# Optimization experiments

Hardware: AMD Instinct MI355X
Metric: run time of the kernel (lower is better)

The kernel has to match this reference:

```python
import jax, jax.numpy as jnp
import numpy as np


def _dF(field, c):
    """Central differences of component c of field [B,X,Y,Z,C] -> [B,X-2,Y-2,Z-2,3]."""
    f = field[..., c]
    dx = (f[:, 2:, 1:-1, 1:-1] - f[:, :-2, 1:-1, 1:-1]) * 0.5
    dy = (f[:, 1:-1, 2:, 1:-1] - f[:, 1:-1, :-2, 1:-1]) * 0.5
    dz = (f[:, 1:-1, 1:-1, 2:] - f[:, 1:-1, 1:-1, :-2]) * 0.5
    return jnp.stack((dx, dy, dz), axis=4)


def setup_inputs() -> dict:
    key = jax.random.key(0)
    grid = jax.random.normal(key, (2, 160, 160, 160, 3), dtype=jnp.float32)
    return {"grid": grid}


def reference(grid):
    # First derivatives of each displacement component: [B,X-2,Y-2,Z-2,3]
    dx = _dF(grid, 0)
    dy = _dF(grid, 1)
    dz = _dF(grid, 2)
    # Second derivatives: [B,X-4,Y-4,Z-4,3]
    dxx = _dF(dx, 0)
    dyy = _dF(dy, 1)
    dzz = _dF(dz, 2)
    dxy = _dF(dx, 1)
    dyz = _dF(dy, 2)
    dxz = _dF(dx, 2)
    penalty = jnp.sum(dxx ** 2 + dyy ** 2 + dzz ** 2
                      + 2.0 * (dxy ** 2 + dyz ** 2 + dxz ** 2))
    return penalty / dxx.size
```

## Files before the change

kernel.cpp:

```cpp
#include <hip/hip_runtime.h>

#define OY 480
#define OX 76800
#define SB 12288000
#define IT 12
#define NSEG 13
#define NBLK 1014
#define INV_SIZE (1.0f/22778496.0f)

#define ROW_SHL1 0x101
#define ROW_SHL2 0x102
#define ROW_SHR1 0x111
#define ROW_SHR2 0x112

template<int CTRL>
__device__ __forceinline__ float dppf(float x){
    return __int_as_float(__builtin_amdgcn_update_dpp(
        0, __float_as_int(x), CTRL, 0xF, 0xF, true));
}

__device__ __forceinline__ float4 ld4p(const float* p){ return *reinterpret_cast<const float4*>(p); }

#define STEP(P, V0a, V0b, DP, WC, WN) { \
    const int s = 2*d + (P); \
    if (qact) { \
        if (s <= 14) { \
            WN[0]=ld4p(nx);    WN[1]=ld4p(nx+4);  WN[2]=ld4p(nx+8); \
            WN[3]=ld4p(nx+12); WN[4]=ld4p(nx+16); WN[5]=ld4p(nx+20); \
            nx += OX; \
        } \
        float x[24]; \
        _Pragma("unroll") for (int q=0;q<6;++q){ \
            x[4*q]=WC[q].x; x[4*q+1]=WC[q].y; x[4*q+2]=WC[q].z; x[4*q+3]=WC[q].w; } \
        float dz0[4], dz1[4], dz2[4], dy0[4], dy1[4], v0c[4]; \
        _Pragma("unroll") for (int v=0; v<4; ++v) { \
            v0c[v] = x[3*v+6]; \
            dz0[v] = x[3*v+9]  - x[3*v+3]; \
            dz1[v] = x[3*v+10] - x[3*v+4]; \
            dz2[v] = x[3*v+11] - x[3*v+5]; \
            dy0[v] = dppf<ROW_SHR1>(x[3*v+6]) - dppf<ROW_SHL1>(x[3*v+6]); \
            dy1[v] = dppf<ROW_SHR1>(x[3*v+7]) - dppf<ROW_SHL1>(x[3*v+7]); \
        } \
        if (s >= 2 && s <= 13) { \
            _Pragma("unroll") for (int v=0; v<4; ++v) { \
                float c0 = x[3*v+6], c1 = x[3*v+7]; \
                float hy0 = dppf<ROW_SHR2>(c0) - 2.f*c0 + dppf<ROW_SHL2>(c0); \
                float hy1 = dppf<ROW_SHR2>(c1) - 2.f*c1 + dppf<ROW_SHL2>(c1); \
                float yz0 = dppf<ROW_SHR1>(dz0[v]) - dppf<ROW_SHL1>(dz0[v]); \
                float yz1 = dppf<ROW_SHR1>(dz1[v]) - dppf<ROW_SHL1>(dz1[v]); \
                float yz2 = dppf<ROW_SHR1>(dz2[v]) - dppf<ROW_SHL1>(dz2[v]); \
                if (vr) { \
                    float zz0 = x[3*v+12] - 2.f*x[3*v+6] + x[3*v]; \
                    float zz1 = x[3*v+13] - 2.f*x[3*v+7] + x[3*v+1]; \
                    float zz2 = x[3*v+14] - 2.f*x[3*v+8] + x[3*v+2]; \
                    cls2 = fmaf(zz0,zz0,cls2); cls2 = fmaf(zz1,zz1,cls2); cls1 = fmaf(zz2,zz2,cls1); \
                    cls2 = fmaf(hy0,hy0,cls2); cls1 = fmaf(hy1,hy1,cls1); \
                    cls4 = fmaf(yz0,yz0,cls4); cls3 = fmaf(yz1,yz1,cls3); cls1 = fmaf(yz2,yz2,cls1); \
                } \
            } \
        } \
        const bool eXY = vr && (s >= 3) && (s <= 14); \
        const bool eXX = vr && (s >= 4); \
        _Pragma("unroll") for (int v=0; v<4; ++v) { \
            if (eXY) { float h; \
                h = dy0[v] - DP[0][v]; cls3 = fmaf(h,h,cls3); \
                h = dy1[v] - DP[1][v]; cls1 = fmaf(h,h,cls1); \
                h = dz0[v] - DP[2][v]; cls3 = fmaf(h,h,cls3); \
                h = dz1[v] - DP[3][v]; cls2 = fmaf(h,h,cls2); \
                h = dz2[v] - DP[4][v]; cls1 = fmaf(h,h,cls1); \
            } \
            DP[0][v] = dy0[v]; DP[1][v] = dy1[v]; \
            DP[2][v] = dz0[v]; DP[3][v] = dz1[v]; DP[4][v] = dz2[v]; \
            if (eXX) { float h = v0c[v] - 2.f*V0a[v] + V0b[v]; cls1 = fmaf(h,h,cls1); } \
            V0b[v] = V0a[v]; V0a[v] = v0c[v]; \
        } \
    } \
}

__global__ __launch_bounds__(256)
void be_partials(const float* __restrict__ g, float* __restrict__ partial) {
    __shared__ float wsum[4];

    const int tid = threadIdx.x;
    const int bid = blockIdx.x;
    const int is = bid % NSEG;
    int r1 = bid / NSEG;
    const int zt = r1 % 3;  r1 /= 3;
    const int jt = r1 % 13;
    const int bb = r1 / 13;

    const int j0  = 2 + jt*12;
    const int zlo = 64*zt;
    const int i0  = 2 + is*IT;
    const float* __restrict__ G = g + (size_t)bb*SB + (size_t)(j0-2)*OY + 3*zlo;

    const int r = tid & 15;
    const int Q = tid >> 4;
    const int qmax = (zt == 2) ? 7 : 16;
    const bool qact = Q < qmax;
    const bool vr = (r >= 2) && (r <= 13);
    const float* lane0 = G + (size_t)r*OY + 12*Q;
    const float* nx = lane0 + (size_t)(i0-1)*OX;

    float4 wA[6], wB[6];
    float v0A0[4], v0A1[4], v0B0[4], v0B1[4];
    float dpA[5][4], dpB[5][4];
    #pragma unroll
    for (int v=0; v<4; ++v) {
        v0A0[v]=v0A1[v]=v0B0[v]=v0B1[v]=0.f;
        #pragma unroll
        for (int q=0; q<5; ++q) { dpA[q][v]=0.f; dpB[q][v]=0.f; }
    }
    float cls1=0.f, cls2=0.f, cls3=0.f, cls4=0.f;

    if (qact) {
        const float* wp = lane0 + (size_t)(i0-2)*OX;
        wA[0]=ld4p(wp);    wA[1]=ld4p(wp+4);  wA[2]=ld4p(wp+8);
        wA[3]=ld4p(wp+12); wA[4]=ld4p(wp+16); wA[5]=ld4p(wp+20);
    }

    #pragma unroll 1
    for (int d = 0; d < 8; ++d) {
        STEP(0, v0A0, v0A1, dpA, wA, wB)
        STEP(1, v0B0, v0B1, dpB, wB, wA)
    }

    float sv = fmaf(2.f, cls2, cls1);
    sv = fmaf(3.f, cls3, sv);
    sv = fmaf(4.f, cls4, sv);
    sv *= 0.0625f;

    #pragma unroll
    for (int off = 32; off > 0; off >>= 1) sv += __shfl_down(sv, off, 64);
    if ((tid & 63) == 0) wsum[tid >> 6] = sv;
    __syncthreads();
    if (tid == 0)
        partial[bid] = (wsum[0] + wsum[1]) + (wsum[2] + wsum[3]);
}

__global__ __launch_bounds__(256)
void be_final(const float* __restrict__ partial, float* __restrict__ out) {
    float s = 0.0f;
    for (int i = threadIdx.x; i < NBLK; i += 256) s += partial[i];
    #pragma unroll
    for (int off = 32; off > 0; off >>= 1) s += __shfl_down(s, off, 64);
    __shared__ float ws[4];
    if ((threadIdx.x & 63) == 0) ws[threadIdx.x >> 6] = s;
    __syncthreads();
    if (threadIdx.x == 0)
        out[0] = ((ws[0] + ws[1]) + (ws[2] + ws[3])) * INV_SIZE;
}

extern "C" void kernel_launch(void* const* d_in, const int* in_sizes, int n_in,
                              void* d_out, int out_size, void* d_ws, size_t ws_size,
                              hipStream_t stream) {
    const float* grid = (const float*)d_in[0];
    float* out = (float*)d_out;
    float* partials = (float*)d_ws;

    be_partials<<<dim3(NBLK), dim3(256), 0, stream>>>(grid, partials);
    be_final<<<1, 256, 0, stream>>>(partials, out);
}
```

Baseline: 166.8 us.

## Stage grid slices through triple-buffered LDS with coalesced loads in single-wave blocks

Each block becomes a single 64-thread wave over a narrower z-window, with 3380 blocks instead of 1014. Each X-slice is fetched with coalesced float4 loads, prefetched one slice ahead in registers and written into a three-slot LDS ring. The stencil then reads its overlapping 24-float windows from LDS rather than issuing redundant overlapping global loads. The slice loop is fully unrolled and the cross-wave shared-memory reduction is dropped. The design relies on in-order LDS access within one wavefront instead of barriers, and it adds LDS traffic plus a larger partials array.

```diff
diff --git a/kernel.cpp b/kernel.cpp
--- a/kernel.cpp
+++ b/kernel.cpp
@@ -3,9 +3,11 @@
 #define OY 480
 #define OX 76800
 #define SB 12288000
+#define RST 60
+#define SLC 960
 #define IT 12
 #define NSEG 13
-#define NBLK 1014
+#define NBLK 3380
 #define INV_SIZE (1.0f/22778496.0f)
 
 #define ROW_SHL1 0x101
@@ -20,90 +22,102 @@
 }
 
 __device__ __forceinline__ float4 ld4p(const float* p){ return *reinterpret_cast<const float4*>(p); }
+__device__ __forceinline__ void st4p(float* p, float4 v){ *reinterpret_cast<float4*>(p) = v; }
 
-#define STEP(P, V0a, V0b, DP, WC, WN) { \
-    const int s = 2*d + (P); \
+#define STEPX(S, V0a, V0b, DP, SBc, SBn) { \
+    if ((S) <= 13) { \
+        const float* bp = Gs + (size_t)((S)+2)*OX; \
+        SBn[0]=ld4p(bp+gof0); SBn[1]=ld4p(bp+gof1); SBn[2]=ld4p(bp+gof2); \
+        if (wv3) SBn[3]=ld4p(bp+gof3); \
+    } \
     if (qact) { \
-        if (s <= 14) { \
-            WN[0]=ld4p(nx);    WN[1]=ld4p(nx+4);  WN[2]=ld4p(nx+8); \
-            WN[3]=ld4p(nx+12); WN[4]=ld4p(nx+16); WN[5]=ld4p(nx+20); \
-            nx += OX; \
-        } \
+        const float* Lr = lds + ((S)%3)*SLC + oj; \
         float x[24]; \
-        _Pragma("unroll") for (int q=0;q<6;++q){ \
-            x[4*q]=WC[q].x; x[4*q+1]=WC[q].y; x[4*q+2]=WC[q].z; x[4*q+3]=WC[q].w; } \
-        float dz0[4], dz1[4], dz2[4], dy0[4], dy1[4], v0c[4]; \
+        { float4 y0=ld4p(Lr),y1=ld4p(Lr+4),y2=ld4p(Lr+8),y3=ld4p(Lr+12),y4=ld4p(Lr+16),y5=ld4p(Lr+20); \
+          x[0]=y0.x;x[1]=y0.y;x[2]=y0.z;x[3]=y0.w; x[4]=y1.x;x[5]=y1.y;x[6]=y1.z;x[7]=y1.w; \
+          x[8]=y2.x;x[9]=y2.y;x[10]=y2.z;x[11]=y2.w; x[12]=y3.x;x[13]=y3.y;x[14]=y3.z;x[15]=y3.w; \
+          x[16]=y4.x;x[17]=y4.y;x[18]=y4.z;x[19]=y4.w; x[20]=y5.x;x[21]=y5.y;x[22]=y5.z;x[23]=y5.w; } \
+        float dz0[4],dz1[4],dz2[4],dy0[4],dy1[4],v0c[4]; \
         _Pragma("unroll") for (int v=0; v<4; ++v) { \
             v0c[v] = x[3*v+6]; \
-            dz0[v] = x[3*v+9]  - x[3*v+3]; \
-            dz1[v] = x[3*v+10] - x[3*v+4]; \
-            dz2[v] = x[3*v+11] - x[3*v+5]; \
+            dz0[v] = x[3*v+9]-x[3*v+3]; dz1[v]=x[3*v+10]-x[3*v+4]; dz2[v]=x[3*v+11]-x[3*v+5]; \
             dy0[v] = dppf<ROW_SHR1>(x[3*v+6]) - dppf<ROW_SHL1>(x[3*v+6]); \
             dy1[v] = dppf<ROW_SHR1>(x[3*v+7]) - dppf<ROW_SHL1>(x[3*v+7]); \
         } \
-        if (s >= 2 && s <= 13) { \
+        if ((S) >= 2 && (S) <= 13) { \
             _Pragma("unroll") for (int v=0; v<4; ++v) { \
-                float c0 = x[3*v+6], c1 = x[3*v+7]; \
+                float c0=x[3*v+6], c1=x[3*v+7]; \
                 float hy0 = dppf<ROW_SHR2>(c0) - 2.f*c0 + dppf<ROW_SHL2>(c0); \
                 float hy1 = dppf<ROW_SHR2>(c1) - 2.f*c1 + dppf<ROW_SHL2>(c1); \
                 float yz0 = dppf<ROW_SHR1>(dz0[v]) - dppf<ROW_SHL1>(dz0[v]); \
                 float yz1 = dppf<ROW_SHR1>(dz1[v]) - dppf<ROW_SHL1>(dz1[v]); \
                 float yz2 = dppf<ROW_SHR1>(dz2[v]) - dppf<ROW_SHL1>(dz2[v]); \
                 if (vr) { \
-                    float zz0 = x[3*v+12] - 2.f*x[3*v+6] + x[3*v]; \
-                    float zz1 = x[3*v+13] - 2.f*x[3*v+7] + x[3*v+1]; \
-                    float zz2 = x[3*v+14] - 2.f*x[3*v+8] + x[3*v+2]; \
-                    cls2 = fmaf(zz0,zz0,cls2); cls2 = fmaf(zz1,zz1,cls2); cls1 = fmaf(zz2,zz2,cls1); \
-                    cls2 = fmaf(hy0,hy0,cls2); cls1 = fmaf(hy1,hy1,cls1); \
-                    cls4 = fmaf(yz0,yz0,cls4); cls3 = fmaf(yz1,yz1,cls3); cls1 = fmaf(yz2,yz2,cls1); \
+                    float zz0 = x[3*v+12]-2.f*x[3*v+6]+x[3*v]; \
+                    float zz1 = x[3*v+13]-2.f*x[3*v+7]+x[3*v+1]; \
+                    float zz2 = x[3*v+14]-2.f*x[3*v+8]+x[3*v+2]; \
+                    cls2=fmaf(zz0,zz0,cls2); cls2=fmaf(zz1,zz1,cls2); cls1=fmaf(zz2,zz2,cls1); \
+                    cls2=fmaf(hy0,hy0,cls2); cls1=fmaf(hy1,hy1,cls1); \
+                    cls4=fmaf(yz0,yz0,cls4); cls3=fmaf(yz1,yz1,cls3); cls1=fmaf(yz2,yz2,cls1); \
                 } \
             } \
         } \
-        const bool eXY = vr && (s >= 3) && (s <= 14); \
-        const bool eXX = vr && (s >= 4); \
         _Pragma("unroll") for (int v=0; v<4; ++v) { \
-            if (eXY) { float h; \
-                h = dy0[v] - DP[0][v]; cls3 = fmaf(h,h,cls3); \
-                h = dy1[v] - DP[1][v]; cls1 = fmaf(h,h,cls1); \
-                h = dz0[v] - DP[2][v]; cls3 = fmaf(h,h,cls3); \
-                h = dz1[v] - DP[3][v]; cls2 = fmaf(h,h,cls2); \
-                h = dz2[v] - DP[4][v]; cls1 = fmaf(h,h,cls1); \
+            if (vr && (S) >= 3 && (S) <= 14) { float h; \
+                h=dy0[v]-DP[0][v]; cls3=fmaf(h,h,cls3); \
+                h=dy1[v]-DP[1][v]; cls1=fmaf(h,h,cls1); \
+                h=dz0[v]-DP[2][v]; cls3=fmaf(h,h,cls3); \
+                h=dz1[v]-DP[3][v]; cls2=fmaf(h,h,cls2); \
+                h=dz2[v]-DP[4][v]; cls1=fmaf(h,h,cls1); \
             } \
-            DP[0][v] = dy0[v]; DP[1][v] = dy1[v]; \
-            DP[2][v] = dz0[v]; DP[3][v] = dz1[v]; DP[4][v] = dz2[v]; \
-            if (eXX) { float h = v0c[v] - 2.f*V0a[v] + V0b[v]; cls1 = fmaf(h,h,cls1); } \
-            V0b[v] = V0a[v]; V0a[v] = v0c[v]; \
+            DP[0][v]=dy0[v]; DP[1][v]=dy1[v]; DP[2][v]=dz0[v]; DP[3][v]=dz1[v]; DP[4][v]=dz2[v]; \
+            if (vr && (S) >= 4) { float h = v0c[v]-2.f*V0a[v]+V0b[v]; cls1=fmaf(h,h,cls1); } \
+            V0b[v]=V0a[v]; V0a[v]=v0c[v]; \
         } \
+    } \
+    if ((S) <= 14) { \
+        float* Lw = lds + (((S)+1)%3)*SLC; \
+        st4p(Lw+lof0, SBc[0]); st4p(Lw+lof1, SBc[1]); st4p(Lw+lof2, SBc[2]); \
+        if (wv3) st4p(Lw+lof3, SBc[3]); \
     } \
 }
 
-__global__ __launch_bounds__(256)
+__global__ __launch_bounds__(64)
 void be_partials(const float* __restrict__ g, float* __restrict__ partial) {
-    __shared__ float wsum[4];
+    __shared__ float lds[3*SLC];
 
     const int tid = threadIdx.x;
     const int bid = blockIdx.x;
     const int is = bid % NSEG;
     int r1 = bid / NSEG;
-    const int zt = r1 % 3;  r1 /= 3;
+    const int zt = r1 % 10; r1 /= 10;
     const int jt = r1 % 13;
     const int bb = r1 / 13;
 
-    const int j0  = 2 + jt*12;
-    const int zlo = 64*zt;
-    const int i0  = 2 + is*IT;
-    const float* __restrict__ G = g + (size_t)bb*SB + (size_t)(j0-2)*OY + 3*zlo;
+    const int j0 = 2 + jt*12;
+    const int wb = (zt < 9) ? 48*zt : 420;
+    const int i0 = 2 + is*IT;
+    const float* __restrict__ Gs =
+        g + (size_t)bb*SB + (size_t)(j0-2)*OY + wb + (size_t)(i0-2)*OX;
+
+    int gof0,gof1,gof2,gof3,lof0,lof1,lof2,lof3;
+    { int f,row,pos;
+      f=tid;     row=f/15; pos=f-15*row; gof0=row*OY+4*pos; lof0=row*RST+4*pos;
+      f=tid+64;  row=f/15; pos=f-15*row; gof1=row*OY+4*pos; lof1=row*RST+4*pos;
+      f=tid+128; row=f/15; pos=f-15*row; gof2=row*OY+4*pos; lof2=row*RST+4*pos;
+      f=tid+192; row=f/15; pos=f-15*row; gof3=row*OY+4*pos; lof3=row*RST+4*pos; }
+    const bool wv3 = tid < 48;
+    if (!wv3) { gof3 = gof0; lof3 = lof0; }
 
     const int r = tid & 15;
     const int Q = tid >> 4;
-    const int qmax = (zt == 2) ? 7 : 16;
+    const int qmax = (zt == 9) ? 3 : 4;
     const bool qact = Q < qmax;
     const bool vr = (r >= 2) && (r <= 13);
-    const float* lane0 = G + (size_t)r*OY + 12*Q;
-    const float* nx = lane0 + (size_t)(i0-1)*OX;
+    const int oj = r*RST + 12*Q + ((zt == 9) ? 12 : 0);
 
-    float4 wA[6], wB[6];
-    float v0A0[4], v0A1[4], v0B0[4], v0B1[4];
+    float4 sA[4], sB[4];
+    float v0A0[4],v0A1[4],v0B0[4],v0B1[4];
     float dpA[5][4], dpB[5][4];
     #pragma unroll
     for (int v=0; v<4; ++v) {
@@ -113,17 +127,29 @@
     }
     float cls1=0.f, cls2=0.f, cls3=0.f, cls4=0.f;
 
-    if (qact) {
-        const float* wp = lane0 + (size_t)(i0-2)*OX;
-        wA[0]=ld4p(wp);    wA[1]=ld4p(wp+4);  wA[2]=ld4p(wp+8);
-        wA[3]=ld4p(wp+12); wA[4]=ld4p(wp+16); wA[5]=ld4p(wp+20);
-    }
+    { float4 a0=ld4p(Gs+gof0), a1=ld4p(Gs+gof1), a2=ld4p(Gs+gof2);
+      st4p(lds+lof0,a0); st4p(lds+lof1,a1); st4p(lds+lof2,a2);
+      if (wv3) { float4 a3=ld4p(Gs+gof3); st4p(lds+lof3,a3); } }
+    { const float* bp = Gs + OX;
+      sB[0]=ld4p(bp+gof0); sB[1]=ld4p(bp+gof1); sB[2]=ld4p(bp+gof2);
+      if (wv3) sB[3]=ld4p(bp+gof3); }
 
-    #pragma unroll 1
-    for (int d = 0; d < 8; ++d) {
-        STEP(0, v0A0, v0A1, dpA, wA, wB)
-        STEP(1, v0B0, v0B1, dpB, wB, wA)
-    }
+    STEPX( 0, v0A0,v0A1,dpA, sB, sA)
+    STEPX( 1, v0B0,v0B1,dpB, sA, sB)
+    STEPX( 2, v0A0,v0A1,dpA, sB, sA)
+    STEPX( 3, v0B0,v0B1,dpB, sA, sB)
+    STEPX( 4, v0A0,v0A1,dpA, sB, sA)
+    STEPX( 5, v0B0,v0B1,dpB, sA, sB)
+    STEPX( 6, v0A0,v0A1,dpA, sB, sA)
+    STEPX( 7, v0B0,v0B1,dpB, sA, sB)
+    STEPX( 8, v0A0,v0A1,dpA, sB, sA)
+    STEPX( 9, v0B0,v0B1,dpB, sA, sB)
+    STEPX(10, v0A0,v0A1,dpA, sB, sA)
+    STEPX(11, v0B0,v0B1,dpB, sA, sB)
+    STEPX(12, v0A0,v0A1,dpA, sB, sA)
+    STEPX(13, v0B0,v0B1,dpB, sA, sB)
+    STEPX(14, v0A0,v0A1,dpA, sB, sA)
+    STEPX(15, v0B0,v0B1,dpB, sA, sB)
 
     float sv = fmaf(2.f, cls2, cls1);
     sv = fmaf(3.f, cls3, sv);
@@ -132,10 +158,7 @@
 
     #pragma unroll
     for (int off = 32; off > 0; off >>= 1) sv += __shfl_down(sv, off, 64);
-    if ((tid & 63) == 0) wsum[tid >> 6] = sv;
-    __syncthreads();
-    if (tid == 0)
-        partial[bid] = (wsum[0] + wsum[1]) + (wsum[2] + wsum[3]);
+    if (tid == 0) partial[bid] = sv;
 }
 
 __global__ __launch_bounds__(256)
@@ -158,6 +181,6 @@
     float* out = (float*)d_out;
     float* partials = (float*)d_ws;
 
-    be_partials<<<dim3(NBLK), dim3(256), 0, stream>>>(grid, partials);
+    be_partials<<<dim3(NBLK), dim3(64), 0, stream>>>(grid, partials);
     be_final<<<1, 256, 0, stream>>>(partials, out);
 }
```

New measurement: 156.1 us. -6.4%, faster.
